# Kernel optimization log

Hardware: AMD Instinct MI355X
Metric: run time of the kernel (lower is better)

Reference implementation:

```python
import jax, jax.numpy as jnp
from jax import lax
import numpy as np

RADIUS = 5
ITERATION = 10
IMG_SHAPE = (2048, 2048, 3)


def make_side_window_kernels(r):
    # 8 directional side-window box kernels, each (2r+1)x(2r+1), minus identity at center
    k = np.ones((2 * r + 1, 1), dtype=np.float64) / (2 * r + 1)
    k_L = k.copy()
    k_L[r + 1:] = 0
    k_L = k_L / np.sum(k_L)
    k_R = k_L[::-1, :]

    def get_kernel(a, b):
        # repeat(a, K, axis=1) * repeat(b.T, K, axis=0) == outer(a, b)
        ab = a @ b.T
        ab = ab.copy()
        ab[r, r] -= 1.0  # residual form: filter - identity
        return ab

    kernel = np.stack([
        get_kernel(k_L, k_L), get_kernel(k_L, k_R),
        get_kernel(k_R, k_L), get_kernel(k_R, k_R),
        get_kernel(k_L, k), get_kernel(k_R, k),
        get_kernel(k, k_L), get_kernel(k, k_R),
    ]).astype(np.float32)
    return kernel[:, np.newaxis, :, :]  # (8, 1, K, K) OIHW


def setup_inputs() -> dict:
    key = jax.random.key(0)
    img = jax.random.uniform(key, IMG_SHAPE, dtype=jnp.float32)
    kernel = jnp.asarray(make_side_window_kernels(RADIUS))
    return {"img": img, "kernel": kernel}


def reference(img, kernel):
    r = RADIUS
    # edge-pad once (numpy 'edge' == jnp 'edge')
    U0 = jnp.pad(img, ((r, r), (r, r), (0, 0)), mode="edge")  # (Hp, Wp, C)

    def step(U, _):
        x = jnp.transpose(U, (2, 0, 1))[:, None]  # (C, 1, Hp, Wp)
        # cross-correlation with zero padding r (matches torch Conv2d padding=r)
        d = lax.conv_general_dilated(x, kernel, (1, 1), [(r, r), (r, r)])  # (C, 8, Hp, Wp)
        idx = jnp.argmin(jnp.abs(d), axis=1, keepdims=True)  # (C, 1, Hp, Wp)
        dm = jnp.take_along_axis(d, idx, axis=1)[:, 0]        # (C, Hp, Wp)
        return U + jnp.transpose(dm, (1, 2, 0)), None

    U, _ = lax.scan(step, U0, None, length=ITERATION)
    return U[r:-r, r:-r, :]
```

## Files before the change

kernel.cpp:

```cpp
#include <hip/hip_runtime.h>

#define H 2048
#define W 2048
#define C 3
#define RAD 5
#define P (H + 2*RAD)
#define RS 2064
#define PLANE ((size_t)P * RS)
#define NITER 10

#define BX 64
#define BY 16
#define EX (BX + 2*RAD)
#define EY (BY + 2*RAD)
#define LSTR (EX + 1)

__global__ void pad_kernel(const float* __restrict__ img, float* __restrict__ dst, int c) {
    int idx = blockIdx.x * blockDim.x + threadIdx.x;
    int total = P * P;
    if (idx >= total) return;
    int y = idx / P;
    int x = idx - y * P;
    int ys = min(max(y - RAD, 0), H - 1);
    int xs = min(max(x - RAD, 0), W - 1);
    dst[(size_t)y * RS + x] = img[((size_t)ys * W + xs) * C + c];
}

__global__ __launch_bounds__(256)
void step_kernel(const float* __restrict__ src, float* __restrict__ dst,
                 const float* __restrict__ kern) {
    __shared__ float sU[EY][LSTR];

    const float w36 = kern[0];
    const float c36 = kern[5 * 11 + 5];
    const float w66 = kern[4 * 121];
    const float c66 = kern[4 * 121 + 5 * 11 + 5];

    const int x0 = blockIdx.x * BX;
    const int y0 = blockIdx.y * BY;
    const int tid = threadIdx.y * 64 + threadIdx.x;

    for (int i = tid; i < EY * EX; i += 256) {
        int r   = i / EX;
        int col = i - r * EX;
        int gy = y0 - RAD + r;
        int gx = x0 - RAD + col;
        float v = 0.0f;
        if (gy >= 0 && gy < P && gx >= 0 && gx < P)
            v = src[(size_t)gy * RS + gx];
        sU[r][col] = v;
    }
    __syncthreads();

    const int tx = threadIdx.x;
    const int gx = x0 + tx;
    const bool xok = (gx < P);

    #pragma unroll 1
    for (int rr = threadIdx.y; rr < BY; rr += 4) {
        int gy = y0 + rr;
        if (!xok || gy >= P) continue;

        float a0 = 0.f, a1 = 0.f, a2 = 0.f, a3 = 0.f;
        float a4 = 0.f, a5 = 0.f, a6 = 0.f, a7 = 0.f;

        #pragma unroll
        for (int ky = 0; ky < 11; ++ky) {
            #pragma unroll
            for (int kx = 0; kx < 11; ++kx) {
                const float uv = sU[rr + ky][tx + kx];
                const bool Lv = (ky <= 5), Rv = (ky >= 5);
                const bool Lh = (kx <= 5), Rh = (kx >= 5);
                const bool ctr = (ky == 5) && (kx == 5);
                const float wc = ctr ? c36 : w36;
                const float ws = ctr ? c66 : w66;
                if (Lv && Lh) a0 = __fadd_rn(a0, __fmul_rn(wc, uv));
                if (Lv && Rh) a1 = __fadd_rn(a1, __fmul_rn(wc, uv));
                if (Rv && Lh) a2 = __fadd_rn(a2, __fmul_rn(wc, uv));
                if (Rv && Rh) a3 = __fadd_rn(a3, __fmul_rn(wc, uv));
                if (Lv)       a4 = __fadd_rn(a4, __fmul_rn(ws, uv));
                if (Rv)       a5 = __fadd_rn(a5, __fmul_rn(ws, uv));
                if (Lh)       a6 = __fadd_rn(a6, __fmul_rn(ws, uv));
                if (Rh)       a7 = __fadd_rn(a7, __fmul_rn(ws, uv));
            }
        }

        float best = a0, ba = fabsf(a0);
        float t;
        t = fabsf(a1); if (t < ba) { ba = t; best = a1; }
        t = fabsf(a2); if (t < ba) { ba = t; best = a2; }
        t = fabsf(a3); if (t < ba) { ba = t; best = a3; }
        t = fabsf(a4); if (t < ba) { ba = t; best = a4; }
        t = fabsf(a5); if (t < ba) { ba = t; best = a5; }
        t = fabsf(a6); if (t < ba) { ba = t; best = a6; }
        t = fabsf(a7); if (t < ba) { ba = t; best = a7; }

        const float u = sU[rr + RAD][tx + RAD];
        dst[(size_t)gy * RS + gx] = __fadd_rn(u, best);
    }
}

__global__ void crop_kernel(const float* __restrict__ src, float* __restrict__ dst, int c) {
    int idx = blockIdx.x * blockDim.x + threadIdx.x;
    int total = H * W;
    if (idx >= total) return;
    int y = idx / W;
    int x = idx - y * W;
    dst[((size_t)y * W + x) * C + c] = src[(size_t)(y + RAD) * RS + (x + RAD)];
}

extern "C" void kernel_launch(void* const* d_in, const int* in_sizes, int n_in,
                              void* d_out, int out_size, void* d_ws, size_t ws_size,
                              hipStream_t stream) {
    const float* img  = (const float*)d_in[0];
    const float* kern = (const float*)d_in[1];
    float* out = (float*)d_out;

    float* b0 = (float*)d_ws;
    float* b1 = b0 + PLANE;

    dim3 sgrid((P + BX - 1) / BX, (P + BY - 1) / BY, 1);
    dim3 sblock(64, 4, 1);

    for (int c = 0; c < C; ++c) {
        {
            int total = P * P;
            pad_kernel<<<(total + 255) / 256, 256, 0, stream>>>(img, b0, c);
        }
        for (int i = 0; i < NITER; ++i) {
            const float* s = (i & 1) ? b1 : b0;
            float*       d = (i & 1) ? b0 : b1;
            step_kernel<<<sgrid, sblock, 0, stream>>>(s, d, kern);
        }
        {
            int total = H * W;
            crop_kernel<<<(total + 255) / 256, 256, 0, stream>>>(b0, out, c);
        }
    }
}
```

Before: 1.917 ms.

## Compute four pixels per thread with float4 windows and batch channels

```diff
diff --git a/kernel.cpp b/kernel.cpp
--- a/kernel.cpp
+++ b/kernel.cpp
@@ -1,4 +1,5 @@
 #include <hip/hip_runtime.h>
+
 
 #define H 2048
 #define W 2048
@@ -9,36 +10,52 @@
 #define PLANE ((size_t)P * RS)
 #define NITER 10
 
-#define BX 64
-#define BY 16
+#define BX 128
+#define BY 8
 #define EX (BX + 2*RAD)
 #define EY (BY + 2*RAD)
-#define LSTR (EX + 1)
+#define LSX 144
 
-__global__ void pad_kernel(const float* __restrict__ img, float* __restrict__ dst, int c) {
+__global__ void pad_kernel(const float* __restrict__ img, float* __restrict__ dst) {
     int idx = blockIdx.x * blockDim.x + threadIdx.x;
-    int total = P * P;
+    int total = C * P * P;
     if (idx >= total) return;
-    int y = idx / P;
-    int x = idx - y * P;
+    int c = idx / (P * P);
+    int rem = idx - c * (P * P);
+    int y = rem / P;
+    int x = rem - y * P;
     int ys = min(max(y - RAD, 0), H - 1);
     int xs = min(max(x - RAD, 0), W - 1);
-    dst[(size_t)y * RS + x] = img[((size_t)ys * W + xs) * C + c];
+    dst[c * PLANE + (size_t)y * RS + x] = img[((size_t)ys * W + xs) * C + c];
+}
+
+__device__ __forceinline__ float select8(const float* a) {
+    float best = a[0], ba = fabsf(a[0]), t;
+    t = fabsf(a[1]); if (t < ba) { ba = t; best = a[1]; }
+    t = fabsf(a[2]); if (t < ba) { ba = t; best = a[2]; }
+    t = fabsf(a[3]); if (t < ba) { ba = t; best = a[3]; }
+    t = fabsf(a[4]); if (t < ba) { ba = t; best = a[4]; }
+    t = fabsf(a[5]); if (t < ba) { ba = t; best = a[5]; }
+    t = fabsf(a[6]); if (t < ba) { ba = t; best = a[6]; }
+    t = fabsf(a[7]); if (t < ba) { ba = t; best = a[7]; }
+    return best;
 }
 
 __global__ __launch_bounds__(256)
 void step_kernel(const float* __restrict__ src, float* __restrict__ dst,
                  const float* __restrict__ kern) {
-    __shared__ float sU[EY][LSTR];
+    __shared__ __align__(16) float sU[EY][LSX];
 
     const float w36 = kern[0];
     const float c36 = kern[5 * 11 + 5];
     const float w66 = kern[4 * 121];
     const float c66 = kern[4 * 121 + 5 * 11 + 5];
 
+    const int ch = blockIdx.z;
+    const float* plane = src + (size_t)ch * PLANE;
     const int x0 = blockIdx.x * BX;
     const int y0 = blockIdx.y * BY;
-    const int tid = threadIdx.y * 64 + threadIdx.x;
+    const int tid = threadIdx.y * 32 + threadIdx.x;
 
     for (int i = tid; i < EY * EX; i += 256) {
         int r   = i / EX;
@@ -47,66 +64,85 @@
         int gx = x0 - RAD + col;
         float v = 0.0f;
         if (gy >= 0 && gy < P && gx >= 0 && gx < P)
-            v = src[(size_t)gy * RS + gx];
+            v = plane[(size_t)gy * RS + gx];
         sU[r][col] = v;
     }
     __syncthreads();
 
-    const int tx = threadIdx.x;
-    const int gx = x0 + tx;
-    const bool xok = (gx < P);
+    const int r   = threadIdx.y;
+    const int X   = threadIdx.x * 4;
+    const int gy  = y0 + r;
+    const int gx0 = x0 + X;
 
-    #pragma unroll 1
-    for (int rr = threadIdx.y; rr < BY; rr += 4) {
-        int gy = y0 + rr;
-        if (!xok || gy >= P) continue;
+    float acc[4][8];
+    #pragma unroll
+    for (int p = 0; p < 4; ++p)
+        #pragma unroll
+        for (int i = 0; i < 8; ++i) acc[p][i] = 0.0f;
+    float uc[4] = {0.f, 0.f, 0.f, 0.f};
 
-        float a0 = 0.f, a1 = 0.f, a2 = 0.f, a3 = 0.f;
-        float a4 = 0.f, a5 = 0.f, a6 = 0.f, a7 = 0.f;
+    #pragma unroll
+    for (int ky = 0; ky < 11; ++ky) {
+        const float4* prow = reinterpret_cast<const float4*>(&sU[r + ky][X]);
+        float4 q0 = prow[0], q1 = prow[1], q2 = prow[2], q3 = prow[3];
+        float win[14];
+        win[0]=q0.x;  win[1]=q0.y;  win[2]=q0.z;  win[3]=q0.w;
+        win[4]=q1.x;  win[5]=q1.y;  win[6]=q1.z;  win[7]=q1.w;
+        win[8]=q2.x;  win[9]=q2.y;  win[10]=q2.z; win[11]=q2.w;
+        win[12]=q3.x; win[13]=q3.y;
+
+        if (ky == 5) { uc[0]=win[5]; uc[1]=win[6]; uc[2]=win[7]; uc[3]=win[8]; }
 
         #pragma unroll
-        for (int ky = 0; ky < 11; ++ky) {
+        for (int kx = 0; kx < 11; ++kx) {
+            const bool Lv = (ky <= 5), Rv = (ky >= 5);
+            const bool Lh = (kx <= 5), Rh = (kx >= 5);
+            const bool ctr = (ky == 5) && (kx == 5);
+            const float wc = ctr ? c36 : w36;
+            const float ws = ctr ? c66 : w66;
             #pragma unroll
-            for (int kx = 0; kx < 11; ++kx) {
-                const float uv = sU[rr + ky][tx + kx];
-                const bool Lv = (ky <= 5), Rv = (ky >= 5);
-                const bool Lh = (kx <= 5), Rh = (kx >= 5);
-                const bool ctr = (ky == 5) && (kx == 5);
-                const float wc = ctr ? c36 : w36;
-                const float ws = ctr ? c66 : w66;
-                if (Lv && Lh) a0 = __fadd_rn(a0, __fmul_rn(wc, uv));
-                if (Lv && Rh) a1 = __fadd_rn(a1, __fmul_rn(wc, uv));
-                if (Rv && Lh) a2 = __fadd_rn(a2, __fmul_rn(wc, uv));
-                if (Rv && Rh) a3 = __fadd_rn(a3, __fmul_rn(wc, uv));
-                if (Lv)       a4 = __fadd_rn(a4, __fmul_rn(ws, uv));
-                if (Rv)       a5 = __fadd_rn(a5, __fmul_rn(ws, uv));
-                if (Lh)       a6 = __fadd_rn(a6, __fmul_rn(ws, uv));
-                if (Rh)       a7 = __fadd_rn(a7, __fmul_rn(ws, uv));
+            for (int p = 0; p < 4; ++p) {
+                const float uv = win[kx + p];
+                if (Lv && Lh) acc[p][0] = __fmaf_rn(wc, uv, acc[p][0]);
+                if (Lv && Rh) acc[p][1] = __fmaf_rn(wc, uv, acc[p][1]);
+                if (Rv && Lh) acc[p][2] = __fmaf_rn(wc, uv, acc[p][2]);
+                if (Rv && Rh) acc[p][3] = __fmaf_rn(wc, uv, acc[p][3]);
+                if (Lv)       acc[p][4] = __fmaf_rn(ws, uv, acc[p][4]);
+                if (Rv)       acc[p][5] = __fmaf_rn(ws, uv, acc[p][5]);
+                if (Lh)       acc[p][6] = __fmaf_rn(ws, uv, acc[p][6]);
+                if (Rh)       acc[p][7] = __fmaf_rn(ws, uv, acc[p][7]);
             }
         }
+    }
 
-        float best = a0, ba = fabsf(a0);
-        float t;
-        t = fabsf(a1); if (t < ba) { ba = t; best = a1; }
-        t = fabsf(a2); if (t < ba) { ba = t; best = a2; }
-        t = fabsf(a3); if (t < ba) { ba = t; best = a3; }
-        t = fabsf(a4); if (t < ba) { ba = t; best = a4; }
-        t = fabsf(a5); if (t < ba) { ba = t; best = a5; }
-        t = fabsf(a6); if (t < ba) { ba = t; best = a6; }
-        t = fabsf(a7); if (t < ba) { ba = t; best = a7; }
+    if (gy < P) {
+        float r0 = __fadd_rn(uc[0], select8(acc[0]));
+        float r1 = __fadd_rn(uc[1], select8(acc[1]));
+        float r2 = __fadd_rn(uc[2], select8(acc[2]));
+        float r3 = __fadd_rn(uc[3], select8(acc[3]));
 
-        const float u = sU[rr + RAD][tx + RAD];
-        dst[(size_t)gy * RS + gx] = __fadd_rn(u, best);
+        float* drow = dst + (size_t)ch * PLANE + (size_t)gy * RS;
+        if (gx0 + 3 < P) {
+            float4 o; o.x = r0; o.y = r1; o.z = r2; o.w = r3;
+            *reinterpret_cast<float4*>(drow + gx0) = o;
+        } else {
+            if (gx0     < P) drow[gx0]     = r0;
+            if (gx0 + 1 < P) drow[gx0 + 1] = r1;
+            if (gx0 + 2 < P) drow[gx0 + 2] = r2;
+            if (gx0 + 3 < P) drow[gx0 + 3] = r3;
+        }
     }
 }
 
-__global__ void crop_kernel(const float* __restrict__ src, float* __restrict__ dst, int c) {
+__global__ void crop_kernel(const float* __restrict__ src, float* __restrict__ dst) {
     int idx = blockIdx.x * blockDim.x + threadIdx.x;
-    int total = H * W;
+    int total = H * W * C;
     if (idx >= total) return;
-    int y = idx / W;
-    int x = idx - y * W;
-    dst[((size_t)y * W + x) * C + c] = src[(size_t)(y + RAD) * RS + (x + RAD)];
+    int tmp = idx / C;
+    int c = idx - tmp * C;
+    int y = tmp / W;
+    int x = tmp - y * W;
+    dst[idx] = src[(size_t)c * PLANE + (size_t)(y + RAD) * RS + (x + RAD)];
 }
 
 extern "C" void kernel_launch(void* const* d_in, const int* in_sizes, int n_in,
@@ -117,24 +153,23 @@
     float* out = (float*)d_out;
 
     float* b0 = (float*)d_ws;
-    float* b1 = b0 + PLANE;
+    float* b1 = b0 + (size_t)C * PLANE;
 
-    dim3 sgrid((P + BX - 1) / BX, (P + BY - 1) / BY, 1);
-    dim3 sblock(64, 4, 1);
+    {
+        int total = C * P * P;
+        pad_kernel<<<(total + 255) / 256, 256, 0, stream>>>(img, b0);
+    }
 
-    for (int c = 0; c < C; ++c) {
-        {
-            int total = P * P;
-            pad_kernel<<<(total + 255) / 256, 256, 0, stream>>>(img, b0, c);
-        }
-        for (int i = 0; i < NITER; ++i) {
-            const float* s = (i & 1) ? b1 : b0;
-            float*       d = (i & 1) ? b0 : b1;
-            step_kernel<<<sgrid, sblock, 0, stream>>>(s, d, kern);
-        }
-        {
-            int total = H * W;
-            crop_kernel<<<(total + 255) / 256, 256, 0, stream>>>(b0, out, c);
-        }
+    dim3 sgrid((P + BX - 1) / BX, (P + BY - 1) / BY, C);
+    dim3 sblock(32, 8, 1);
+    for (int i = 0; i < NITER; ++i) {
+        const float* s = (i & 1) ? b1 : b0;
+        float*       d = (i & 1) ? b0 : b1;
+        step_kernel<<<sgrid, sblock, 0, stream>>>(s, d, kern);
+    }
+
+    {
+        int total = H * W * C;
+        crop_kernel<<<(total + 255) / 256, 256, 0, stream>>>(b0, out);
     }
 }
```

Measured after the change: 2.642 ms. 1.38x slower.
